# Kernel tuning notes

Measured on AMD Instinct MI355X. Metric: run time of the kernel, lower is better.

Reference implementation:

```python
import jax, jax.numpy as jnp
import numpy as np

N = 1024      # side of the square relation matrix
K = 64        # in_dim
OUT = 64      # out_dim
N_W = 15      # h_params_asym


def setup_inputs() -> dict:
    key = jax.random.key(0)
    k1, k2 = jax.random.split(key)
    S = N * N
    input_layer = jax.random.normal(k1, (S, K), dtype=jnp.float32)
    stdv = 1.0 / float(np.sqrt(K))
    weights = jax.random.uniform(k2, (N_W, K, OUT), minval=-stdv, maxval=stdv, dtype=jnp.float32)
    ar = jnp.arange(S, dtype=jnp.int32)
    rows = ar // N                       # row index of each flattened entry
    cols = ar % N                        # col index of each flattened entry
    idx_trans = cols * N + rows          # transpose permutation
    idx_diag = jnp.arange(N, dtype=jnp.int32) * (N + 1)  # diagonal positions
    idx_all = jnp.zeros((S,), dtype=jnp.int32)           # single segment
    idx_diag_broad = jnp.zeros((N,), dtype=jnp.int32)    # pool diag to one segment
    col_norm = jnp.full((N,), float(N), dtype=jnp.float32)   # each column-segment has N members
    row_norm = jnp.full((N,), float(N), dtype=jnp.float32)
    all_norm = jnp.array([float(S)], dtype=jnp.float32)
    diag_norm = jnp.array([float(N)], dtype=jnp.float32)
    return dict(input_layer=input_layer, weights=weights,
                idx_trans=idx_trans, idx_diag=idx_diag, idx_row=rows, idx_col=cols,
                idx_all=idx_all, idx_diag_broad=idx_diag_broad,
                col_norm=col_norm, row_norm=row_norm, all_norm=all_norm, diag_norm=diag_norm)


def reference(input_layer, weights, idx_trans, idx_diag, idx_row, idx_col,
              idx_all, idx_diag_broad, col_norm, row_norm, all_norm, diag_norm):
    S = input_layer.shape[0]
    n = idx_diag.shape[0]
    out_dim = weights.shape[2]

    def pool(X, idx, norm, nseg):
        # normalized segment mean (index_add then divide)
        return jax.ops.segment_sum(X, idx, num_segments=nseg) / norm[:, None]

    def scatter_diag(X):
        # scatter n rows onto the diagonal positions of an [S, out_dim] zero tensor
        return jnp.zeros((S, out_dim), X.dtype).at[idx_diag].set(X)

    transpose = input_layer[idx_trans]            # [S, k]
    diagonal = input_layer[idx_diag]              # [n, k]
    row_pool = pool(input_layer, idx_col, col_norm, n)   # [n, k]
    col_pool = pool(input_layer, idx_row, row_norm, n)   # [n, k]
    all_pool = pool(input_layer, idx_all, all_norm, 1)   # [1, k]
    diag_pool = pool(diagonal, idx_diag_broad, diag_norm, 1)  # [1, k]

    output = input_layer @ weights[0]
    output += transpose @ weights[1]
    output += scatter_diag(diagonal @ weights[2])
    output += (row_pool @ weights[3])[idx_col]    # row_pool broadcast over col idx
    output += (row_pool @ weights[4])[idx_row]    # row_pool broadcast over row idx
    output += (col_pool @ weights[5])[idx_row]
    output += (col_pool @ weights[6])[idx_col]
    output += (all_pool @ weights[7])[idx_all]
    output += scatter_diag((diag_pool @ weights[8])[idx_diag_broad])
    output += scatter_diag((all_pool @ weights[9])[idx_diag_broad])
    output += scatter_diag(row_pool @ weights[10])
    output += scatter_diag(col_pool @ weights[11])
    output += (diag_pool @ weights[12])[idx_all]
    output += (diagonal @ weights[13])[idx_col]
    output += (diagonal @ weights[14])[idx_row]
    return output
```

## Files before the change

kernel.cpp:

```cpp
#include <hip/hip_runtime.h>
#include <hip/hip_bf16.h>

typedef __attribute__((ext_vector_type(8))) short short8;
typedef __attribute__((ext_vector_type(4))) float floatx4;

__device__ __forceinline__ unsigned short f2bf(float f) {
    __hip_bfloat16 h = __float2bfloat16(f);
    return __builtin_bit_cast(unsigned short, h);
}

__device__ __forceinline__ short8 cvt2x4(floatx4 a, floatx4 b) {
    short8 v;
    v[0] = (short)f2bf(a[0]); v[1] = (short)f2bf(a[1]);
    v[2] = (short)f2bf(a[2]); v[3] = (short)f2bf(a[3]);
    v[4] = (short)f2bf(b[0]); v[5] = (short)f2bf(b[1]);
    v[6] = (short)f2bf(b[2]); v[7] = (short)f2bf(b[3]);
    return v;
}

__global__ __launch_bounds__(256) void sweep_kernel(const float* __restrict__ in,
        float* __restrict__ rowpart, float* __restrict__ colpart) {
    __shared__ float col_lds[64][64];
    __shared__ float rowp[4][16][64];
    int t = threadIdx.x;
    int lane = t & 63, w = t >> 6;
    int kq = lane & 15, cg = lane >> 4;
    int c0 = blockIdx.x * 16;
    int r0 = blockIdx.y * 64;

    floatx4 rowacc[4];
    #pragma unroll
    for (int cl = 0; cl < 4; ++cl) rowacc[cl] = (floatx4){0.f, 0.f, 0.f, 0.f};

    #pragma unroll 4
    for (int i = 0; i < 16; ++i) {
        int rloc = w + 4 * i;
        const float* p = in + ((size_t)(r0 + rloc) << 16) + (size_t)c0 * 64 + cg * 64 + kq * 4;
        floatx4 v0 = *(const floatx4*)(p);
        floatx4 v1 = *(const floatx4*)(p + 256);
        floatx4 v2 = *(const floatx4*)(p + 512);
        floatx4 v3 = *(const floatx4*)(p + 768);
        rowacc[0] += v0; rowacc[1] += v1; rowacc[2] += v2; rowacc[3] += v3;
        floatx4 cs = v0 + v1 + v2 + v3;
        #pragma unroll
        for (int m = 16; m <= 32; m <<= 1) {
            cs[0] += __shfl_xor(cs[0], m);
            cs[1] += __shfl_xor(cs[1], m);
            cs[2] += __shfl_xor(cs[2], m);
            cs[3] += __shfl_xor(cs[3], m);
        }
        if (cg == 0) *(floatx4*)&col_lds[rloc][kq * 4] = cs;
    }
    #pragma unroll
    for (int cl = 0; cl < 4; ++cl)
        *(floatx4*)&rowp[w][cg + 4 * cl][kq * 4] = rowacc[cl];
    __syncthreads();

    #pragma unroll
    for (int q = 0; q < 4; ++q) {
        int idx = q * 256 + t;
        int rloc = idx >> 4, kq2 = idx & 15;
        floatx4 v = *(const floatx4*)&col_lds[rloc][kq2 * 4];
        *(floatx4*)&colpart[(size_t)blockIdx.x * 65536 + (size_t)(r0 + rloc) * 64 + kq2 * 4] = v;
    }
    {
        int c = t >> 4, kq2 = t & 15;
        floatx4 s = *(const floatx4*)&rowp[0][c][kq2 * 4];
        s += *(const floatx4*)&rowp[1][c][kq2 * 4];
        s += *(const floatx4*)&rowp[2][c][kq2 * 4];
        s += *(const floatx4*)&rowp[3][c][kq2 * 4];
        *(floatx4*)&rowpart[(size_t)blockIdx.y * 65536 + (size_t)(c0 + c) * 64 + kq2 * 4] = s;
    }
}

__global__ __launch_bounds__(256) void rowfin_kernel(const float* __restrict__ rowpart,
        float* __restrict__ row_pool) {
    int j = blockIdx.x * 256 + threadIdx.x;
    const floatx4* rp4 = (const floatx4*)rowpart;
    floatx4 s = (floatx4){0.f, 0.f, 0.f, 0.f};
    #pragma unroll
    for (int y = 0; y < 16; ++y) s += rp4[(size_t)y * 16384 + j];
    s *= (1.f / 1024.f);
    *(floatx4*)&row_pool[j * 4] = s;
}

__global__ __launch_bounds__(256) void colfin_kernel(const float* __restrict__ colpart,
        float* __restrict__ col_pool, float* __restrict__ allraw) {
    __shared__ float red[16][64];
    int t = threadIdx.x;
    int j = blockIdx.x * 256 + t;
    const floatx4* cp4 = (const floatx4*)colpart;
    floatx4 s = (floatx4){0.f, 0.f, 0.f, 0.f};
    #pragma unroll 8
    for (int y = 0; y < 64; ++y) s += cp4[(size_t)y * 16384 + j];
    *(floatx4*)&col_pool[j * 4] = s * (1.f / 1024.f);
    int rloc = t >> 4, kq = t & 15;
    *(floatx4*)&red[rloc][kq * 4] = s;
    __syncthreads();
    if (t < 64) {
        float a = 0.f;
        #pragma unroll
        for (int q = 0; q < 16; ++q) a += red[q][t];
        atomicAdd(&allraw[t], a);
    }
}

__global__ __launch_bounds__(256) void diag_kernel(const float* __restrict__ in,
        float* __restrict__ diagbuf, float* __restrict__ diagraw) {
    __shared__ float red[4][64];
    int t = threadIdx.x, k = t & 63, il = t >> 6;
    int i = blockIdx.x * 4 + il;
    float v = in[(size_t)i * 65600 + k];
    diagbuf[i * 64 + k] = v;
    red[il][k] = v;
    __syncthreads();
    if (t < 64)
        atomicAdd(&diagraw[t], red[0][t] + red[1][t] + red[2][t] + red[3][t]);
}

__global__ __launch_bounds__(256) void wconv_kernel(const float* __restrict__ wts,
        unsigned short* __restrict__ w0t, unsigned short* __restrict__ w1t) {
    int idx = blockIdx.x * 256 + threadIdx.x;
    int n = idx >> 6, k = idx & 63;
    w0t[idx] = f2bf(wts[k * 64 + n]);
    w1t[idx] = f2bf(wts[4096 + k * 64 + n]);
}

__global__ __launch_bounds__(256) void abd_kernel(const float* __restrict__ W,
        const float* __restrict__ col_pool, const float* __restrict__ row_pool,
        const float* __restrict__ diagbuf, const float* __restrict__ allraw,
        const float* __restrict__ diagraw,
        float* __restrict__ Ab, float* __restrict__ Bb, float* __restrict__ Dgb) {
    __shared__ float rp[8][64], cp[8][64], dv[8][64], ap[64], dp[64];
    int t = threadIdx.x, o = t & 63, il = t >> 6;
    int i0 = blockIdx.x * 8;
    #pragma unroll
    for (int q = 0; q < 2; ++q) {
        int ii = il + 4 * q;
        rp[ii][o] = row_pool[(i0 + ii) * 64 + o];
        cp[ii][o] = col_pool[(i0 + ii) * 64 + o];
        dv[ii][o] = diagbuf[(i0 + ii) * 64 + o];
    }
    if (t < 64) {
        ap[t] = allraw[t] * (1.f / 1048576.f);
        dp[t] = diagraw[t] * (1.f / 1024.f);
    }
    __syncthreads();
    int iA = il, iB = il + 4;
    float aA0 = 0.f, aA1 = 0.f, aB0 = 0.f, aB1 = 0.f, aD0 = 0.f, aD1 = 0.f;
    float cA = 0.f, cD = 0.f;
    #pragma unroll 4
    for (int k = 0; k < 64; ++k) {
        int ko = k * 64 + o;
        float w2  = W[2 * 4096 + ko],  w3  = W[3 * 4096 + ko];
        float w4  = W[4 * 4096 + ko],  w5  = W[5 * 4096 + ko];
        float w6  = W[6 * 4096 + ko],  w7  = W[7 * 4096 + ko];
        float w8  = W[8 * 4096 + ko],  w9  = W[9 * 4096 + ko];
        float w10 = W[10 * 4096 + ko], w11 = W[11 * 4096 + ko];
        float w12 = W[12 * 4096 + ko], w13 = W[13 * 4096 + ko];
        float w14 = W[14 * 4096 + ko];
        float rA = rp[iA][k], cAk = cp[iA][k], dA = dv[iA][k];
        float rB = rp[iB][k], cBk = cp[iB][k], dB = dv[iB][k];
        aA0 += rA * w3 + cAk * w6 + dA * w13;
        aA1 += rB * w3 + cBk * w6 + dB * w13;
        aB0 += rA * w4 + cAk * w5 + dA * w14;
        aB1 += rB * w4 + cBk * w5 + dB * w14;
        aD0 += dA * w2 + rA * w10 + cAk * w11;
        aD1 += dB * w2 + rB * w10 + cBk * w11;
        cA += ap[k] * w7 + dp[k] * w12;
        cD += dp[k] * w8 + ap[k] * w9;
    }
    Ab[(i0 + iA) * 64 + o]  = aA0 + cA;
    Ab[(i0 + iB) * 64 + o]  = aA1 + cA;
    Bb[(i0 + iA) * 64 + o]  = aB0;
    Bb[(i0 + iB) * 64 + o]  = aB1;
    Dgb[(i0 + iA) * 64 + o] = aD0 + cD;
    Dgb[(i0 + iB) * 64 + o] = aD1 + cD;
}

__global__ __launch_bounds__(256, 2) void main_kernel(const float* __restrict__ in,
        const unsigned short* __restrict__ w0t, const unsigned short* __restrict__ w1t,
        const float* __restrict__ Ab, const float* __restrict__ Bb,
        const float* __restrict__ Dgb, float* __restrict__ out) {
    __shared__ short lds[32768];

    int t = threadIdx.x;
    int lane = t & 63, w = t >> 6;
    int lrow = lane & 15, lhi = lane >> 4;

    int p = blockIdx.x;
    float fb = (129.0f - sqrtf(129.0f * 129.0f - 8.0f * (float)p)) * 0.5f;
    int bi = (int)fb;
    while (bi > 0 && bi * (129 - bi) / 2 > p) --bi;
    while ((bi + 1) * (129 - (bi + 1)) / 2 <= p) ++bi;
    int bj = bi + (p - bi * (129 - bi) / 2);
    int r0 = bi * 16, c0 = bj * 16;

    short8 bw0[2][4], bw1[2][4];
    #pragma unroll
    for (int kg = 0; kg < 2; ++kg)
        #pragma unroll
        for (int nt = 0; nt < 4; ++nt) {
            int off = (nt * 16 + lrow) * 64 + kg * 32 + lhi * 8;
            bw0[kg][nt] = *(const short8*)(w0t + off);
            bw1[kg][nt] = *(const short8*)(w1t + off);
        }

    int sj = (t & 127) >> 3;
    int sg = t & 7;
    int shalf = t >> 7;
    floatx4 st0[16], st1[16];
    #pragma unroll
    for (int q = 0; q < 8; ++q) {
        int i = 2 * q + shalf;
        const float* s0 = in + (((size_t)(r0 + i) << 10) + (c0 + sj)) * 64 + sg * 8;
        st0[2 * q]     = *(const floatx4*)s0;
        st0[2 * q + 1] = *(const floatx4*)(s0 + 4);
    }
    #pragma unroll
    for (int q = 0; q < 8; ++q) {
        int i = 2 * q + shalf;
        const float* s1 = in + (((size_t)(c0 + i) << 10) + (r0 + sj)) * 64 + sg * 8;
        st1[2 * q]     = *(const floatx4*)s1;
        st1[2 * q + 1] = *(const floatx4*)(s1 + 4);
    }
    #pragma unroll
    for (int q = 0; q < 8; ++q) {
        int i = 2 * q + shalf;
        int row = i * 16 + sj;
        int wg = sg ^ ((row ^ (row >> 4)) & 7);
        *(short8*)(lds + row * 64 + wg * 8) = cvt2x4(st0[2 * q], st0[2 * q + 1]);
    }
    #pragma unroll
    for (int q = 0; q < 8; ++q) {
        int i = 2 * q + shalf;
        int row = i * 16 + sj;
        int wg = sg ^ ((row ^ (row >> 4)) & 7);
        *(short8*)(lds + 16384 + row * 64 + wg * 8) = cvt2x4(st1[2 * q], st1[2 * q + 1]);
    }
    __syncthreads();

    #pragma unroll
    for (int sel = 0; sel < 2; ++sel) {
        if (sel == 1 && bi == bj) continue;
        int selb = sel * 16384;
        int othb = (sel ^ 1) * 16384;
        int rbase = sel ? c0 : r0;
        int cbase = sel ? r0 : c0;
        #pragma unroll
        for (int mf = 0; mf < 4; ++mf) {
            int I = w * 4 + mf;
            int mrow = I * 16 + lrow;
            int swzm = (mrow ^ (mrow >> 4)) & 7;
            int trow = lrow * 16 + I;
            int swzt = (trow ^ (trow >> 4)) & 7;
            short8 ad[2], at2[2];
            #pragma unroll
            for (int kg = 0; kg < 2; ++kg) {
                ad[kg]  = *(const short8*)(lds + selb + mrow * 64 + ((kg * 4 + lhi) ^ swzm) * 8);
                at2[kg] = *(const short8*)(lds + othb + trow * 64 + ((kg * 4 + lhi) ^ swzt) * 8);
            }
            floatx4 acc[4];
            #pragma unroll
            for (int nt = 0; nt < 4; ++nt) acc[nt] = (floatx4){0.f, 0.f, 0.f, 0.f};
            #pragma unroll
            for (int nt = 0; nt < 4; ++nt) {
                acc[nt] = __builtin_amdgcn_mfma_f32_16x16x32_bf16(ad[0],  bw0[0][nt], acc[nt], 0, 0, 0);
                acc[nt] = __builtin_amdgcn_mfma_f32_16x16x32_bf16(ad[1],  bw0[1][nt], acc[nt], 0, 0, 0);
                acc[nt] = __builtin_amdgcn_mfma_f32_16x16x32_bf16(at2[0], bw1[0][nt], acc[nt], 0, 0, 0);
                acc[nt] = __builtin_amdgcn_mfma_f32_16x16x32_bf16(at2[1], bw1[1][nt], acc[nt], 0, 0, 0);
            }
            int ridx = rbase + I;
            float br[4];
            #pragma unroll
            for (int nt = 0; nt < 4; ++nt) br[nt] = Bb[ridx * 64 + nt * 16 + lrow];
            #pragma unroll
            for (int jj = 0; jj < 4; ++jj) {
                int j = lhi * 4 + jj;
                int cidx = cbase + j;
                size_t s = ((size_t)ridx << 10) + cidx;
                bool isd = (ridx == cidx);
                #pragma unroll
                for (int nt = 0; nt < 4; ++nt) {
                    int n = nt * 16 + lrow;
                    float v = acc[nt][jj] + Ab[cidx * 64 + n] + br[nt];
                    if (isd) v += Dgb[ridx * 64 + n];
                    out[s * 64 + n] = v;
                }
            }
        }
    }
}

extern "C" void kernel_launch(void* const* d_in, const int* in_sizes, int n_in,
                              void* d_out, int out_size, void* d_ws, size_t ws_size,
                              hipStream_t stream) {
    const float* in  = (const float*)d_in[0];
    const float* wts = (const float*)d_in[1];
    float* out = (float*)d_out;
    float* ws = (float*)d_ws;

    float* colpart  = ws;
    float* rowpart  = ws + 4194304;
    float* row_pool = ws + 5242880;
    float* col_pool = ws + 5308416;
    float* diagbuf  = ws + 5373952;
    float* allraw   = ws + 5439488;
    float* diagraw  = ws + 5439552;
    float* Ab       = ws + 5439616;
    float* Bb       = ws + 5505152;
    float* Dgb      = ws + 5570688;
    unsigned short* w0t = (unsigned short*)(ws + 5636224);
    unsigned short* w1t = w0t + 4096;

    hipMemsetAsync((void*)allraw, 0, 128 * sizeof(float), stream);

    sweep_kernel<<<dim3(64, 16), 256, 0, stream>>>(in, rowpart, colpart);
    rowfin_kernel<<<64, 256, 0, stream>>>(rowpart, row_pool);
    colfin_kernel<<<64, 256, 0, stream>>>(colpart, col_pool, allraw);
    diag_kernel<<<256, 256, 0, stream>>>(in, diagbuf, diagraw);
    wconv_kernel<<<16, 256, 0, stream>>>(wts, w0t, w1t);
    abd_kernel<<<128, 256, 0, stream>>>(wts, col_pool, row_pool, diagbuf,
                                        allraw, diagraw, Ab, Bb, Dgb);
    main_kernel<<<2080, 256, 0, stream>>>(in, w0t, w1t, Ab, Bb, Dgb, out);
}
```

Before: 246.5 us.

## Write swizzled bf16 tile copy in sweep and read it in main kernel

```diff
diff --git a/kernel.cpp b/kernel.cpp
--- a/kernel.cpp
+++ b/kernel.cpp
@@ -1,6 +1,7 @@
 #include <hip/hip_runtime.h>
 #include <hip/hip_bf16.h>
 
+typedef __attribute__((ext_vector_type(4))) short shortx4;
 typedef __attribute__((ext_vector_type(8))) short short8;
 typedef __attribute__((ext_vector_type(4))) float floatx4;
 
@@ -9,39 +10,35 @@
     return __builtin_bit_cast(unsigned short, h);
 }
 
-__device__ __forceinline__ short8 cvt2x4(floatx4 a, floatx4 b) {
-    short8 v;
-    v[0] = (short)f2bf(a[0]); v[1] = (short)f2bf(a[1]);
-    v[2] = (short)f2bf(a[2]); v[3] = (short)f2bf(a[3]);
-    v[4] = (short)f2bf(b[0]); v[5] = (short)f2bf(b[1]);
-    v[6] = (short)f2bf(b[2]); v[7] = (short)f2bf(b[3]);
-    return v;
-}
-
 __global__ __launch_bounds__(256) void sweep_kernel(const float* __restrict__ in,
-        float* __restrict__ rowpart, float* __restrict__ colpart) {
-    __shared__ float col_lds[64][64];
-    __shared__ float rowp[4][16][64];
+        unsigned short* __restrict__ bfcopy, float* __restrict__ rowpart,
+        float* __restrict__ colpart, float* __restrict__ diagbuf) {
+    __shared__ float colp[4][16][64];
     int t = threadIdx.x;
-    int lane = t & 63, w = t >> 6;
-    int kq = lane & 15, cg = lane >> 4;
-    int c0 = blockIdx.x * 16;
-    int r0 = blockIdx.y * 64;
-
-    floatx4 rowacc[4];
-    #pragma unroll
-    for (int cl = 0; cl < 4; ++cl) rowacc[cl] = (floatx4){0.f, 0.f, 0.f, 0.f};
-
-    #pragma unroll 4
+    int kq = t & 15;
+    int cl = (t >> 4) & 3;
+    int w  = t >> 6;
+    int c  = w * 4 + cl;
+    int ti = blockIdx.y, tj = blockIdx.x;
+    int R = ti * 16, C = tj * 16;
+    const float* base = in + ((size_t)R << 16) + (size_t)(C + c) * 64 + kq * 4;
+    unsigned short* tbase = bfcopy + ((size_t)(ti * 64 + tj) << 14);
+    bool dt = (ti == tj);
+
+    floatx4 rowacc = (floatx4){0.f, 0.f, 0.f, 0.f};
+    #pragma unroll
     for (int i = 0; i < 16; ++i) {
-        int rloc = w + 4 * i;
-        const float* p = in + ((size_t)(r0 + rloc) << 16) + (size_t)c0 * 64 + cg * 64 + kq * 4;
-        floatx4 v0 = *(const floatx4*)(p);
-        floatx4 v1 = *(const floatx4*)(p + 256);
-        floatx4 v2 = *(const floatx4*)(p + 512);
-        floatx4 v3 = *(const floatx4*)(p + 768);
-        rowacc[0] += v0; rowacc[1] += v1; rowacc[2] += v2; rowacc[3] += v3;
-        floatx4 cs = v0 + v1 + v2 + v3;
+        floatx4 v = __builtin_nontemporal_load((const floatx4*)(base + ((size_t)i << 16)));
+        rowacc += v;
+        int row = i * 16 + c;
+        int wg = (kq >> 1) ^ ((row ^ (row >> 4)) & 7);
+        shortx4 h;
+        h[0] = (short)f2bf(v[0]); h[1] = (short)f2bf(v[1]);
+        h[2] = (short)f2bf(v[2]); h[3] = (short)f2bf(v[3]);
+        *(shortx4*)(tbase + (size_t)row * 64 + wg * 8 + (kq & 1) * 4) = h;
+        if (dt && c == i)
+            *(floatx4*)&diagbuf[(size_t)(R + i) * 64 + kq * 4] = v;
+        floatx4 cs = v;
         #pragma unroll
         for (int m = 16; m <= 32; m <<= 1) {
             cs[0] += __shfl_xor(cs[0], m);
@@ -49,81 +46,65 @@
             cs[2] += __shfl_xor(cs[2], m);
             cs[3] += __shfl_xor(cs[3], m);
         }
-        if (cg == 0) *(floatx4*)&col_lds[rloc][kq * 4] = cs;
-    }
-    #pragma unroll
-    for (int cl = 0; cl < 4; ++cl)
-        *(floatx4*)&rowp[w][cg + 4 * cl][kq * 4] = rowacc[cl];
+        if (cl == 0) *(floatx4*)&colp[w][i][kq * 4] = cs;
+    }
+    *(floatx4*)&rowpart[(size_t)ti * 65536 + (size_t)(C + c) * 64 + kq * 4] = rowacc;
     __syncthreads();
-
-    #pragma unroll
-    for (int q = 0; q < 4; ++q) {
-        int idx = q * 256 + t;
-        int rloc = idx >> 4, kq2 = idx & 15;
-        floatx4 v = *(const floatx4*)&col_lds[rloc][kq2 * 4];
-        *(floatx4*)&colpart[(size_t)blockIdx.x * 65536 + (size_t)(r0 + rloc) * 64 + kq2 * 4] = v;
-    }
-    {
-        int c = t >> 4, kq2 = t & 15;
-        floatx4 s = *(const floatx4*)&rowp[0][c][kq2 * 4];
-        s += *(const floatx4*)&rowp[1][c][kq2 * 4];
-        s += *(const floatx4*)&rowp[2][c][kq2 * 4];
-        s += *(const floatx4*)&rowp[3][c][kq2 * 4];
-        *(floatx4*)&rowpart[(size_t)blockIdx.y * 65536 + (size_t)(c0 + c) * 64 + kq2 * 4] = s;
-    }
-}
-
-__global__ __launch_bounds__(256) void rowfin_kernel(const float* __restrict__ rowpart,
-        float* __restrict__ row_pool) {
-    int j = blockIdx.x * 256 + threadIdx.x;
-    const floatx4* rp4 = (const floatx4*)rowpart;
-    floatx4 s = (floatx4){0.f, 0.f, 0.f, 0.f};
-    #pragma unroll
-    for (int y = 0; y < 16; ++y) s += rp4[(size_t)y * 16384 + j];
-    s *= (1.f / 1024.f);
-    *(floatx4*)&row_pool[j * 4] = s;
-}
-
-__global__ __launch_bounds__(256) void colfin_kernel(const float* __restrict__ colpart,
-        float* __restrict__ col_pool, float* __restrict__ allraw) {
+    int i2 = t >> 4, kq2 = t & 15;
+    floatx4 s = *(const floatx4*)&colp[0][i2][kq2 * 4];
+    s += *(const floatx4*)&colp[1][i2][kq2 * 4];
+    s += *(const floatx4*)&colp[2][i2][kq2 * 4];
+    s += *(const floatx4*)&colp[3][i2][kq2 * 4];
+    *(floatx4*)&colpart[(size_t)tj * 65536 + (size_t)(R + i2) * 64 + kq2 * 4] = s;
+}
+
+__global__ __launch_bounds__(256) void poolfin_kernel(const float* __restrict__ rowpart,
+        const float* __restrict__ colpart, const float* __restrict__ diagbuf,
+        const float* __restrict__ wts,
+        float* __restrict__ row_pool, float* __restrict__ col_pool,
+        float* __restrict__ allraw, float* __restrict__ diagraw,
+        unsigned short* __restrict__ w0t, unsigned short* __restrict__ w1t) {
     __shared__ float red[16][64];
-    int t = threadIdx.x;
-    int j = blockIdx.x * 256 + t;
-    const floatx4* cp4 = (const floatx4*)colpart;
-    floatx4 s = (floatx4){0.f, 0.f, 0.f, 0.f};
-    #pragma unroll 8
-    for (int y = 0; y < 64; ++y) s += cp4[(size_t)y * 16384 + j];
-    *(floatx4*)&col_pool[j * 4] = s * (1.f / 1024.f);
-    int rloc = t >> 4, kq = t & 15;
-    *(floatx4*)&red[rloc][kq * 4] = s;
-    __syncthreads();
-    if (t < 64) {
-        float a = 0.f;
-        #pragma unroll
-        for (int q = 0; q < 16; ++q) a += red[q][t];
-        atomicAdd(&allraw[t], a);
-    }
-}
-
-__global__ __launch_bounds__(256) void diag_kernel(const float* __restrict__ in,
-        float* __restrict__ diagbuf, float* __restrict__ diagraw) {
-    __shared__ float red[4][64];
-    int t = threadIdx.x, k = t & 63, il = t >> 6;
-    int i = blockIdx.x * 4 + il;
-    float v = in[(size_t)i * 65600 + k];
-    diagbuf[i * 64 + k] = v;
-    red[il][k] = v;
-    __syncthreads();
-    if (t < 64)
-        atomicAdd(&diagraw[t], red[0][t] + red[1][t] + red[2][t] + red[3][t]);
-}
-
-__global__ __launch_bounds__(256) void wconv_kernel(const float* __restrict__ wts,
-        unsigned short* __restrict__ w0t, unsigned short* __restrict__ w1t) {
-    int idx = blockIdx.x * 256 + threadIdx.x;
-    int n = idx >> 6, k = idx & 63;
-    w0t[idx] = f2bf(wts[k * 64 + n]);
-    w1t[idx] = f2bf(wts[4096 + k * 64 + n]);
+    int b = blockIdx.x, t = threadIdx.x;
+    if (b < 64) {
+        int j = b * 256 + t;
+        const floatx4* rp4 = (const floatx4*)rowpart;
+        floatx4 s = (floatx4){0.f, 0.f, 0.f, 0.f};
+        #pragma unroll 8
+        for (int y = 0; y < 64; ++y) s += rp4[(size_t)y * 16384 + j];
+        *(floatx4*)&row_pool[j * 4] = s * (1.f / 1024.f);
+    } else if (b < 128) {
+        int j = (b - 64) * 256 + t;
+        const floatx4* cp4 = (const floatx4*)colpart;
+        floatx4 s = (floatx4){0.f, 0.f, 0.f, 0.f};
+        #pragma unroll 8
+        for (int y = 0; y < 64; ++y) s += cp4[(size_t)y * 16384 + j];
+        *(floatx4*)&col_pool[j * 4] = s * (1.f / 1024.f);
+        *(floatx4*)&red[t >> 4][(t & 15) * 4] = s;
+        __syncthreads();
+        if (t < 64) {
+            float a = 0.f;
+            #pragma unroll
+            for (int q = 0; q < 16; ++q) a += red[q][t];
+            atomicAdd(&allraw[t], a);
+        }
+    } else if (b < 136) {
+        int d = b - 128;
+        int k = t & 63, rl = t >> 6;
+        float sd = 0.f;
+        #pragma unroll 8
+        for (int u = 0; u < 32; ++u)
+            sd += diagbuf[(size_t)(d * 128 + rl + 4 * u) * 64 + k];
+        red[rl][k] = sd;
+        __syncthreads();
+        if (t < 64)
+            atomicAdd(&diagraw[t], red[0][t] + red[1][t] + red[2][t] + red[3][t]);
+    } else {
+        int idx = (b - 136) * 256 + t;
+        int n = idx >> 6, k = idx & 63;
+        w0t[idx] = f2bf(wts[k * 64 + n]);
+        w1t[idx] = f2bf(wts[4096 + k * 64 + n]);
+    }
 }
 
 __global__ __launch_bounds__(256) void abd_kernel(const float* __restrict__ W,
@@ -178,7 +159,7 @@
     Dgb[(i0 + iB) * 64 + o] = aD1 + cD;
 }
 
-__global__ __launch_bounds__(256, 2) void main_kernel(const float* __restrict__ in,
+__global__ __launch_bounds__(256, 2) void main_kernel(const unsigned short* __restrict__ bfcopy,
         const unsigned short* __restrict__ w0t, const unsigned short* __restrict__ w1t,
         const float* __restrict__ Ab, const float* __restrict__ Bb,
         const float* __restrict__ Dgb, float* __restrict__ out) {
@@ -206,37 +187,17 @@
             bw1[kg][nt] = *(const short8*)(w1t + off);
         }
 
-    int sj = (t & 127) >> 3;
-    int sg = t & 7;
-    int shalf = t >> 7;
-    floatx4 st0[16], st1[16];
-    #pragma unroll
-    for (int q = 0; q < 8; ++q) {
-        int i = 2 * q + shalf;
-        const float* s0 = in + (((size_t)(r0 + i) << 10) + (c0 + sj)) * 64 + sg * 8;
-        st0[2 * q]     = *(const floatx4*)s0;
-        st0[2 * q + 1] = *(const floatx4*)(s0 + 4);
-    }
-    #pragma unroll
-    for (int q = 0; q < 8; ++q) {
-        int i = 2 * q + shalf;
-        const float* s1 = in + (((size_t)(c0 + i) << 10) + (r0 + sj)) * 64 + sg * 8;
-        st1[2 * q]     = *(const floatx4*)s1;
-        st1[2 * q + 1] = *(const floatx4*)(s1 + 4);
-    }
-    #pragma unroll
-    for (int q = 0; q < 8; ++q) {
-        int i = 2 * q + shalf;
-        int row = i * 16 + sj;
-        int wg = sg ^ ((row ^ (row >> 4)) & 7);
-        *(short8*)(lds + row * 64 + wg * 8) = cvt2x4(st0[2 * q], st0[2 * q + 1]);
-    }
-    #pragma unroll
-    for (int q = 0; q < 8; ++q) {
-        int i = 2 * q + shalf;
-        int row = i * 16 + sj;
-        int wg = sg ^ ((row ^ (row >> 4)) & 7);
-        *(short8*)(lds + 16384 + row * 64 + wg * 8) = cvt2x4(st1[2 * q], st1[2 * q + 1]);
+    const unsigned short* t0 = bfcopy + ((size_t)(bi * 64 + bj) << 14);
+    const unsigned short* t1 = bfcopy + ((size_t)(bj * 64 + bi) << 14);
+    #pragma unroll
+    for (int n = 0; n < 8; ++n) {
+        int g = n * 256 + t;
+        *(short8*)(lds + g * 8) = *(const short8*)(t0 + g * 8);
+    }
+    #pragma unroll
+    for (int n = 0; n < 8; ++n) {
+        int g = n * 256 + t;
+        *(short8*)(lds + 16384 + g * 8) = *(const short8*)(t1 + g * 8);
     }
     __syncthreads();
 
@@ -285,7 +246,7 @@
                     int n = nt * 16 + lrow;
                     float v = acc[nt][jj] + Ab[cidx * 64 + n] + br[nt];
                     if (isd) v += Dgb[ridx * 64 + n];
-                    out[s * 64 + n] = v;
+                    __builtin_nontemporal_store(v, &out[s * 64 + n]);
                 }
             }
         }
@@ -300,27 +261,26 @@
     float* out = (float*)d_out;
     float* ws = (float*)d_ws;
 
-    float* colpart  = ws;
-    float* rowpart  = ws + 4194304;
-    float* row_pool = ws + 5242880;
-    float* col_pool = ws + 5308416;
-    float* diagbuf  = ws + 5373952;
-    float* allraw   = ws + 5439488;
-    float* diagraw  = ws + 5439552;
-    float* Ab       = ws + 5439616;
-    float* Bb       = ws + 5505152;
-    float* Dgb      = ws + 5570688;
-    unsigned short* w0t = (unsigned short*)(ws + 5636224);
+    unsigned short* bfcopy = (unsigned short*)ws;
+    float* rowpart  = ws + 33554432;
+    float* colpart  = ws + 37748736;
+    float* row_pool = ws + 41943040;
+    float* col_pool = ws + 42008576;
+    float* diagbuf  = ws + 42074112;
+    float* allraw   = ws + 42139648;
+    float* diagraw  = ws + 42139712;
+    float* Ab       = ws + 42139776;
+    float* Bb       = ws + 42205312;
+    float* Dgb      = ws + 42270848;
+    unsigned short* w0t = (unsigned short*)(ws + 42336384);
     unsigned short* w1t = w0t + 4096;
 
-    hipMemsetAsync((void*)allraw, 0, 128 * sizeof(float), stream);
-
-    sweep_kernel<<<dim3(64, 16), 256, 0, stream>>>(in, rowpart, colpart);
-    rowfin_kernel<<<64, 256, 0, stream>>>(rowpart, row_pool);
-    colfin_kernel<<<64, 256, 0, stream>>>(colpart, col_pool, allraw);
-    diag_kernel<<<256, 256, 0, stream>>>(in, diagbuf, diagraw);
-    wconv_kernel<<<16, 256, 0, stream>>>(wts, w0t, w1t);
+    (void)hipMemsetAsync((void*)allraw, 0, 128 * sizeof(float), stream);
+
+    sweep_kernel<<<dim3(64, 64), 256, 0, stream>>>(in, bfcopy, rowpart, colpart, diagbuf);
+    poolfin_kernel<<<152, 256, 0, stream>>>(rowpart, colpart, diagbuf, wts,
+                                            row_pool, col_pool, allraw, diagraw, w0t, w1t);
     abd_kernel<<<128, 256, 0, stream>>>(wts, col_pool, row_pool, diagbuf,
                                         allraw, diagraw, Ab, Bb, Dgb);
-    main_kernel<<<2080, 256, 0, stream>>>(in, w0t, w1t, Ab, Bb, Dgb, out);
-}
+    main_kernel<<<2080, 256, 0, stream>>>(bfcopy, w0t, w1t, Ab, Bb, Dgb, out);
+}
```

Result: faster. 214.3 us (-13.1%).
